# Kernel tuning notes

Measured on AMD Instinct MI355X. Metric: run time of the kernel, lower is better.

## Reference

```python
import jax, jax.numpy as jnp
import numpy as np

H = 64          # hidden_dim
L = 4           # num_layers
N_SENS = 32
OUT_DIM = 3
EPS = 1e-5


def _ln(x, g, b):
    m = jnp.mean(x, axis=-1, keepdims=True)
    v = jnp.var(x, axis=-1, keepdims=True)
    return (x - m) / jnp.sqrt(v + EPS) * g + b


def _gelu(x):
    return jax.nn.gelu(x, approximate=False)  # torch nn.GELU default (erf)


def setup_inputs() -> dict:
    key = jax.random.key(0)
    ks = jax.random.split(key, 12)
    B, T = 512, 2048
    s = 0.05
    return {
        "sensors": jax.random.normal(ks[0], (B, T, N_SENS), dtype=jnp.float32),
        # input_proj: Linear(n_sensors,H), LayerNorm(H), GELU, Linear(H,H)
        "W_in1": jax.random.normal(ks[1], (N_SENS, H), dtype=jnp.float32) * s,
        "b_in1": jnp.zeros((H,), jnp.float32),
        "ln1_g": jnp.ones((H,), jnp.float32),
        "ln1_b": jnp.zeros((H,), jnp.float32),
        "W_in2": jax.random.normal(ks[2], (H, H), dtype=jnp.float32) * s,
        "b_in2": jnp.zeros((H,), jnp.float32),
        # stacked LSTM cell gate weights: Linear(2H, 4H) per layer
        "Wg": jax.random.normal(ks[3], (L, 2 * H, 4 * H), dtype=jnp.float32) * s,
        "bg": jnp.zeros((L, 4 * H), jnp.float32),
        # output_proj: LayerNorm(H), Linear(H,H), GELU, Linear(H,out)
        "ln2_g": jnp.ones((H,), jnp.float32),
        "ln2_b": jnp.zeros((H,), jnp.float32),
        "W_out1": jax.random.normal(ks[4], (H, H), dtype=jnp.float32) * s,
        "b_out1": jnp.zeros((H,), jnp.float32),
        "W_out2": jax.random.normal(ks[5], (H, OUT_DIM), dtype=jnp.float32) * s,
        "b_out2": jnp.zeros((OUT_DIM,), jnp.float32),
    }


def _forward(sensors, W_in1, b_in1, ln1_g, ln1_b, W_in2, b_in2,
             Wg, bg, ln2_g, ln2_b, W_out1, b_out1, W_out2, b_out2):
    B, T, _ = sensors.shape
    # input projection (batched over B,T)
    x = _gelu(_ln(sensors @ W_in1 + b_in1, ln1_g, ln1_b)) @ W_in2 + b_in2  # [B,T,H]
    x_t = jnp.swapaxes(x, 0, 1)  # [T,B,H] for scan over time

    h0 = jnp.zeros((L, B, H), x.dtype)
    c0 = jnp.zeros((L, B, H), x.dtype)

    def step(carry, xt):
        h, c = carry  # [L,B,H]
        inp = xt
        hs, cs = [], []
        for l in range(L):  # fixed small layer loop
            combined = jnp.concatenate([inp, h[l]], axis=-1)  # [B,2H]
            gates = combined @ Wg[l] + bg[l]                   # [B,4H]
            i, f, g, o = jnp.split(gates, 4, axis=-1)
            c_new = jax.nn.sigmoid(f) * c[l] + jax.nn.sigmoid(i) * jnp.tanh(g)
            h_new = jax.nn.sigmoid(o) * jnp.tanh(c_new)
            hs.append(h_new)
            cs.append(c_new)
            inp = h_new
        return (jnp.stack(hs), jnp.stack(cs)), hs[-1]

    _, out_t = jax.lax.scan(step, (h0, c0), x_t)  # out_t: [T,B,H]
    out = jnp.swapaxes(out_t, 0, 1)  # [B,T,H]
    y = _gelu(_ln(out, ln2_g, ln2_b) @ W_out1 + b_out1) @ W_out2 + b_out2
    return y  # [B,T,OUT_DIM]


def reference(sensors, W_in1, b_in1, ln1_g, ln1_b, W_in2, b_in2,
              Wg, bg, ln2_g, ln2_b, W_out1, b_out1, W_out2, b_out2):
    return _forward(sensors, W_in1, b_in1, ln1_g, ln1_b, W_in2, b_in2,
                    Wg, bg, ln2_g, ln2_b, W_out1, b_out1, W_out2, b_out2)
```

## Files before the change

### kernel.cpp

```cpp
#include <hip/hip_runtime.h>
#include <math.h>

#define B_   512
#define T_   2048
#define H_   64
#define NS_  32
#define HH_  128
#define G4_  256
#define EPSF 1e-5f

typedef _Float16 half8 __attribute__((ext_vector_type(8)));
typedef _Float16 h4   __attribute__((ext_vector_type(4)));
typedef float    f32x4 __attribute__((ext_vector_type(4)));

__device__ __forceinline__ float gelu_f(float x) {
    return 0.5f * x * (1.0f + erff(x * 0.70710678118654752440f));
}
__device__ __forceinline__ float sigmoid_f(float x) {
    return 1.0f / (1.0f + __expf(-x));
}
__device__ __forceinline__ float tanh_f(float x) {
    return 1.0f - 2.0f / (__expf(2.0f * x) + 1.0f);
}

__global__ void __launch_bounds__(256) inproj_kernel(
    const float* __restrict__ sensors, const float* __restrict__ W1,
    const float* __restrict__ b1, const float* __restrict__ g1,
    const float* __restrict__ bb1, const float* __restrict__ W2,
    const float* __restrict__ b2, _Float16* __restrict__ seqh)
{
    __shared__ __align__(16) float W1l[NS_ * H_];
    __shared__ __align__(16) float W2l[H_ * H_];
    __shared__ float p1[H_], p2[H_], p3[H_], p4[H_];
    const int tid = threadIdx.x;
    {
        const float4* s1 = (const float4*)W1;
        float4* d1 = (float4*)W1l;
        for (int i = tid; i < NS_ * H_ / 4; i += 256) d1[i] = s1[i];
        const float4* s2 = (const float4*)W2;
        float4* d2 = (float4*)W2l;
        for (int i = tid; i < H_ * H_ / 4; i += 256) d2[i] = s2[i];
        if (tid < H_) { p1[tid] = b1[tid]; p2[tid] = g1[tid];
                        p3[tid] = bb1[tid]; p4[tid] = b2[tid]; }
    }
    __syncthreads();

    const long idx = (long)blockIdx.x * 256 + tid;
    const float* srow = sensors + idx * NS_;
    float sv[NS_];
    #pragma unroll
    for (int q = 0; q < NS_ / 4; ++q) {
        float4 v = *(const float4*)&srow[q * 4];
        sv[q*4+0] = v.x; sv[q*4+1] = v.y; sv[q*4+2] = v.z; sv[q*4+3] = v.w;
    }
    float t1[H_];
    #pragma unroll
    for (int jb = 0; jb < H_ / 4; ++jb) {
        float ax = p1[jb*4+0], ay = p1[jb*4+1], az = p1[jb*4+2], aw = p1[jb*4+3];
        #pragma unroll
        for (int k = 0; k < NS_; ++k) {
            float4 w = *(const float4*)&W1l[k * H_ + jb * 4];
            ax += sv[k]*w.x; ay += sv[k]*w.y; az += sv[k]*w.z; aw += sv[k]*w.w;
        }
        t1[jb*4+0] = ax; t1[jb*4+1] = ay; t1[jb*4+2] = az; t1[jb*4+3] = aw;
    }
    float mean = 0.f;
    #pragma unroll
    for (int j = 0; j < H_; ++j) mean += t1[j];
    mean *= (1.0f / H_);
    float var = 0.f;
    #pragma unroll
    for (int j = 0; j < H_; ++j) { float d = t1[j] - mean; var += d * d; }
    var *= (1.0f / H_);
    const float inv = rsqrtf(var + EPSF);
    #pragma unroll
    for (int j = 0; j < H_; ++j) {
        float nv = (t1[j] - mean) * inv * p2[j] + p3[j];
        t1[j] = gelu_f(nv);
    }
    _Float16* orow = seqh + idx * H_;
    for (int ob = 0; ob < H_ / 4; ++ob) {
        float ax = p4[ob*4+0], ay = p4[ob*4+1];
        float az = p4[ob*4+2], aw = p4[ob*4+3];
        #pragma unroll
        for (int j = 0; j < H_; ++j) {
            float4 w = *(const float4*)&W2l[j * H_ + ob * 4];
            ax += t1[j]*w.x; ay += t1[j]*w.y; az += t1[j]*w.z; aw += t1[j]*w.w;
        }
        h4 o; o[0] = (_Float16)ax; o[1] = (_Float16)ay;
              o[2] = (_Float16)az; o[3] = (_Float16)aw;
        *(h4*)&orow[ob * 4] = o;
    }
}

__global__ void __launch_bounds__(512, 2) lstm_fused_kernel(
    const float* __restrict__ Wg, const float* __restrict__ bg,
    const _Float16* __restrict__ xin,
    _Float16* __restrict__ h3out)
{
    __shared__ __align__(16) _Float16 combh[4][2][HH_];
    __shared__ __align__(8)  float gbuf[4][4][H_][2];

    const int tid  = threadIdx.x;
    const int wv   = tid >> 6;
    const int lane = tid & 63;
    const int l    = wv >> 1;
    const int half = wv & 1;
    const int L    = lane & 15;
    const int kgrp = lane >> 4;

    const float* W = Wg + (size_t)l * HH_ * G4_;
    half8 wf[4][8];
    #pragma unroll
    for (int kt = 0; kt < 4; ++kt) {
        #pragma unroll
        for (int nt = 0; nt < 8; ++nt) {
            const int col = half * 128 + nt * 16 + L;
            half8 f;
            #pragma unroll
            for (int j = 0; j < 8; ++j)
                f[j] = (_Float16)W[(kt * 32 + kgrp * 8 + j) * G4_ + col];
            wf[kt][nt] = f;
        }
    }
    float ba[8];
    #pragma unroll
    for (int nt = 0; nt < 8; ++nt)
        ba[nt] = bg[l * G4_ + half * 128 + nt * 16 + L];

    const int nl_l = tid >> 7;
    const int nrow = (tid >> 6) & 1;
    const int u    = tid & 63;
    const long nbase = ((long)(blockIdx.x * 2 + nrow)) * T_ * H_ + u;

    const int  xrow = lane >> 5;
    const int  xu   = half * 32 + (lane & 31);
    const long xbase = ((long)(blockIdx.x * 2 + xrow)) * T_ * H_ + xu;

    for (int i = tid; i < 4 * 2 * HH_ / 2; i += 512) ((float*)combh)[i] = 0.f;
    __syncthreads();
    if (l == 0) combh[0][xrow][xu] = xin[xbase];
    __syncthreads();

    float c_reg = 0.f;

    for (int s = 0; s < T_ + 3; ++s) {
        const bool mact = (s >= l) && (s - l < T_);
        const bool nact = (s >= nl_l) && (s - nl_l < T_);

        _Float16 xnext = (_Float16)0.f;
        if (l == 0 && s + 1 < T_)
            xnext = xin[xbase + (long)(s + 1) * H_];

        if (mact) {
            const _Float16* cp = &combh[l][lane & 1][0];
            half8 af[4];
            #pragma unroll
            for (int kt = 0; kt < 4; ++kt)
                af[kt] = *(const half8*)&cp[kt * 32 + kgrp * 8];

            f32x4 acc[8];
            #pragma unroll
            for (int nt = 0; nt < 8; ++nt)
                acc[nt] = (f32x4){ba[nt], ba[nt], ba[nt], ba[nt]};
            #pragma unroll
            for (int kt = 0; kt < 4; ++kt) {
                #pragma unroll
                for (int nt = 0; nt < 8; ++nt)
                    acc[nt] = __builtin_amdgcn_mfma_f32_16x16x32_f16(
                        af[kt], wf[kt][nt], acc[nt], 0, 0, 0);
            }
            if (lane < 16) {
                #pragma unroll
                for (int nt = 0; nt < 8; ++nt) {
                    const int col = half * 128 + nt * 16 + lane;
                    const int g   = col >> 6;
                    const int ug  = col & 63;
                    float2 v; v.x = acc[nt][0]; v.y = acc[nt][1];
                    *(float2*)&gbuf[l][g][ug][0] = v;
                }
            }
        }
        __syncthreads();

        if (nact) {
            const int t = s - nl_l;
            const float gi = gbuf[nl_l][0][u][nrow];
            const float gf = gbuf[nl_l][1][u][nrow];
            const float gg = gbuf[nl_l][2][u][nrow];
            const float go = gbuf[nl_l][3][u][nrow];
            c_reg = sigmoid_f(gf) * c_reg + sigmoid_f(gi) * tanh_f(gg);
            const float hn = sigmoid_f(go) * tanh_f(c_reg);
            const _Float16 hh = (_Float16)hn;
            combh[nl_l][nrow][64 + u] = hh;
            if (nl_l < 3) combh[nl_l + 1][nrow][u] = hh;
            else          h3out[nbase + (long)t * H_] = hh;
        }
        if (l == 0 && s + 1 < T_)
            combh[0][xrow][xu] = xnext;
        __syncthreads();
    }
}

__global__ void __launch_bounds__(256) outproj_kernel(
    const _Float16* __restrict__ h16,
    const float* __restrict__ g2, const float* __restrict__ b2,
    const float* __restrict__ W1, const float* __restrict__ b1,
    const float* __restrict__ W2, const float* __restrict__ b2o,
    float* __restrict__ y)
{
    __shared__ __align__(16) float W1l[H_ * H_];
    __shared__ __align__(16) float W2l[H_ * 4];
    __shared__ float pg[H_], pb[H_], pb1[H_];
    const int tid = threadIdx.x;
    {
        const float4* s1 = (const float4*)W1;
        float4* d1 = (float4*)W1l;
        for (int i = tid; i < H_ * H_ / 4; i += 256) d1[i] = s1[i];
        if (tid < H_) {
            pg[tid] = g2[tid]; pb[tid] = b2[tid]; pb1[tid] = b1[tid];
            float4 w; w.x = W2[tid*3+0]; w.y = W2[tid*3+1]; w.z = W2[tid*3+2]; w.w = 0.f;
            *(float4*)&W2l[tid * 4] = w;
        }
    }
    __syncthreads();

    const long idx = (long)blockIdx.x * 256 + tid;
    const _Float16* hrow = h16 + idx * H_;
    float hv[H_];
    #pragma unroll
    for (int q = 0; q < H_ / 8; ++q) {
        half8 v = *(const half8*)&hrow[q * 8];
        #pragma unroll
        for (int j = 0; j < 8; ++j) hv[q*8+j] = (float)v[j];
    }
    float mean = 0.f;
    #pragma unroll
    for (int j = 0; j < H_; ++j) mean += hv[j];
    mean *= (1.0f / H_);
    float var = 0.f;
    #pragma unroll
    for (int j = 0; j < H_; ++j) { float dd = hv[j] - mean; var += dd * dd; }
    var *= (1.0f / H_);
    const float inv = rsqrtf(var + EPSF);
    #pragma unroll
    for (int j = 0; j < H_; ++j) hv[j] = (hv[j] - mean) * inv * pg[j] + pb[j];

    float y0 = b2o[0], y1 = b2o[1], y2 = b2o[2];
    for (int ob = 0; ob < H_ / 4; ++ob) {
        float ax = pb1[ob*4+0], ay = pb1[ob*4+1];
        float az = pb1[ob*4+2], aw = pb1[ob*4+3];
        #pragma unroll
        for (int j = 0; j < H_; ++j) {
            float4 w = *(const float4*)&W1l[j * H_ + ob * 4];
            ax += hv[j]*w.x; ay += hv[j]*w.y; az += hv[j]*w.z; aw += hv[j]*w.w;
        }
        ax = gelu_f(ax); ay = gelu_f(ay); az = gelu_f(az); aw = gelu_f(aw);
        float4 wa = *(const float4*)&W2l[(ob*4+0) * 4];
        float4 wb = *(const float4*)&W2l[(ob*4+1) * 4];
        float4 wc = *(const float4*)&W2l[(ob*4+2) * 4];
        float4 wd = *(const float4*)&W2l[(ob*4+3) * 4];
        y0 += ax*wa.x + ay*wb.x + az*wc.x + aw*wd.x;
        y1 += ax*wa.y + ay*wb.y + az*wc.y + aw*wd.y;
        y2 += ax*wa.z + ay*wb.z + az*wc.z + aw*wd.z;
    }
    y[idx * 3 + 0] = y0;
    y[idx * 3 + 1] = y1;
    y[idx * 3 + 2] = y2;
}

extern "C" void kernel_launch(void* const* d_in, const int* in_sizes, int n_in,
                              void* d_out, int out_size, void* d_ws, size_t ws_size,
                              hipStream_t stream)
{
    const float* sensors = (const float*)d_in[0];
    const float* W_in1   = (const float*)d_in[1];
    const float* b_in1   = (const float*)d_in[2];
    const float* ln1_g   = (const float*)d_in[3];
    const float* ln1_b   = (const float*)d_in[4];
    const float* W_in2   = (const float*)d_in[5];
    const float* b_in2   = (const float*)d_in[6];
    const float* Wg      = (const float*)d_in[7];
    const float* bg      = (const float*)d_in[8];
    const float* ln2_g   = (const float*)d_in[9];
    const float* ln2_b   = (const float*)d_in[10];
    const float* W_out1  = (const float*)d_in[11];
    const float* b_out1  = (const float*)d_in[12];
    const float* W_out2  = (const float*)d_in[13];
    const float* b_out2  = (const float*)d_in[14];
    float* y = (float*)d_out;

    const size_t elems = (size_t)B_ * T_ * H_;
    _Float16* seqh = (_Float16*)d_ws;
    _Float16* h3   = (_Float16*)((char*)d_ws + elems * 2);

    inproj_kernel<<<B_ * T_ / 256, 256, 0, stream>>>(
        sensors, W_in1, b_in1, ln1_g, ln1_b, W_in2, b_in2, seqh);
    lstm_fused_kernel<<<B_ / 2, 512, 0, stream>>>(Wg, bg, seqh, h3);
    outproj_kernel<<<B_ * T_ / 256, 256, 0, stream>>>(
        h3, ln2_g, ln2_b, W_out1, b_out1, W_out2, b_out2, y);
}
```

Baseline: 3.082 ms.

## Split LSTM gate GEMM across 16 waves and stage x/h through chunked rings

The LSTM block grows from 512 to 1024 threads, so each layer's gate GEMM is split across four waves of 64 columns each instead of two waves of 128. That halves the per-wave MFMA chain on the serial critical path. Input x is now prefetched in 8-timestep chunks into a double-buffered shared ring with 16-byte loads. Layer-3 outputs are collected in a ring and written out in 16-byte vector stores by dedicated waves, replacing per-step scalar global loads and stores. The risks are heavier 1024-thread __syncthreads barriers on every step, lower occupancy per CU, and more shared memory.

```diff
diff --git a/kernel.cpp b/kernel.cpp
--- a/kernel.cpp
+++ b/kernel.cpp
@@ -93,112 +93,143 @@
     }
 }
 
-__global__ void __launch_bounds__(512, 2) lstm_fused_kernel(
+__global__ void __launch_bounds__(1024, 4) lstm_fused_kernel(
     const float* __restrict__ Wg, const float* __restrict__ bg,
     const _Float16* __restrict__ xin,
     _Float16* __restrict__ h3out)
 {
     __shared__ __align__(16) _Float16 combh[4][2][HH_];
-    __shared__ __align__(8)  float gbuf[4][4][H_][2];
+    __shared__ __align__(16) float    gbuf[4][2][4][H_];
+    __shared__ __align__(16) _Float16 xring[2][2][8][H_];
+    __shared__ __align__(16) _Float16 hring[2][2][8][H_];
 
     const int tid  = threadIdx.x;
     const int wv   = tid >> 6;
     const int lane = tid & 63;
-    const int l    = wv >> 1;
-    const int half = wv & 1;
+    const int l    = wv >> 2;
+    const int q    = wv & 3;
     const int L    = lane & 15;
     const int kgrp = lane >> 4;
+    const int arow = lane & 1;
 
     const float* W = Wg + (size_t)l * HH_ * G4_;
-    half8 wf[4][8];
+    half8 wf[4][4];
     #pragma unroll
     for (int kt = 0; kt < 4; ++kt) {
         #pragma unroll
-        for (int nt = 0; nt < 8; ++nt) {
-            const int col = half * 128 + nt * 16 + L;
+        for (int nt = 0; nt < 4; ++nt) {
             half8 f;
             #pragma unroll
             for (int j = 0; j < 8; ++j)
-                f[j] = (_Float16)W[(kt * 32 + kgrp * 8 + j) * G4_ + col];
+                f[j] = (_Float16)W[(kt * 32 + kgrp * 8 + j) * G4_
+                                   + q * 64 + nt * 16 + L];
             wf[kt][nt] = f;
         }
     }
-    float ba[8];
-    #pragma unroll
-    for (int nt = 0; nt < 8; ++nt)
-        ba[nt] = bg[l * G4_ + half * 128 + nt * 16 + L];
-
-    const int nl_l = tid >> 7;
-    const int nrow = (tid >> 6) & 1;
-    const int u    = tid & 63;
-    const long nbase = ((long)(blockIdx.x * 2 + nrow)) * T_ * H_ + u;
-
-    const int  xrow = lane >> 5;
-    const int  xu   = half * 32 + (lane & 31);
-    const long xbase = ((long)(blockIdx.x * 2 + xrow)) * T_ * H_ + xu;
-
-    for (int i = tid; i < 4 * 2 * HH_ / 2; i += 512) ((float*)combh)[i] = 0.f;
+    float ba[4];
+    #pragma unroll
+    for (int nt = 0; nt < 4; ++nt)
+        ba[nt] = bg[l * G4_ + q * 64 + nt * 16 + L];
+
+    const bool nlw  = tid < 512;
+    const int  nl_l = tid >> 7;
+    const int  nrow = (tid >> 6) & 1;
+    const int  u    = tid & 63;
+
+    const int xt  = lane >> 3;
+    const int xu8 = (lane & 7) * 8;
+
+    const bool xw   = (wv < 2);
+    const int  xrow = wv & 1;
+    const _Float16* xsrc =
+        xin + ((long)(blockIdx.x * 2 + xrow)) * T_ * H_ + xt * H_ + xu8;
+
+    const bool hw   = (wv >= 14);
+    const int  hrow = hw ? (wv - 14) : 0;
+    _Float16* hdst =
+        h3out + ((long)(blockIdx.x * 2 + hrow)) * T_ * H_ + xt * H_ + xu8;
+
+    if (tid < 512) ((float*)combh)[tid] = 0.f;
+    half8 xreg = {};
+    if (xw) xreg = *(const half8*)xsrc;
     __syncthreads();
-    if (l == 0) combh[0][xrow][xu] = xin[xbase];
+    if (xw) {
+        *(half8*)&xring[0][xrow][xt][xu8] = xreg;
+        xreg = *(const half8*)(xsrc + 8 * H_);
+    }
     __syncthreads();
 
     float c_reg = 0.f;
 
     for (int s = 0; s < T_ + 3; ++s) {
+        if (xw && (s & 7) == 0) {
+            const int c = s >> 3;
+            if (c + 1 < T_ / 8)
+                *(half8*)&xring[(c + 1) & 1][xrow][xt][xu8] = xreg;
+            if (c + 2 < T_ / 8)
+                xreg = *(const half8*)(xsrc + (long)(c + 2) * 8 * H_);
+        }
+        if (hw && s >= 11 && ((s - 3) & 7) == 0) {
+            const int cp = ((s - 3) >> 3) - 1;
+            half8 v = *(const half8*)&hring[cp & 1][hrow][xt][xu8];
+            *(half8*)(hdst + (long)cp * 8 * H_) = v;
+        }
+
         const bool mact = (s >= l) && (s - l < T_);
-        const bool nact = (s >= nl_l) && (s - nl_l < T_);
-
-        _Float16 xnext = (_Float16)0.f;
-        if (l == 0 && s + 1 < T_)
-            xnext = xin[xbase + (long)(s + 1) * H_];
-
         if (mact) {
-            const _Float16* cp = &combh[l][lane & 1][0];
-            half8 af[4];
+            const _Float16* px = (l == 0)
+                ? &xring[(s >> 3) & 1][arow][s & 7][0]
+                : &combh[l][arow][0];
+            const _Float16* ph = &combh[l][arow][64];
+            half8 af0 = *(const half8*)(px + kgrp * 8);
+            half8 af1 = *(const half8*)(px + 32 + kgrp * 8);
+            half8 af2 = *(const half8*)(ph + kgrp * 8);
+            half8 af3 = *(const half8*)(ph + 32 + kgrp * 8);
+
+            f32x4 acc[4];
             #pragma unroll
-            for (int kt = 0; kt < 4; ++kt)
-                af[kt] = *(const half8*)&cp[kt * 32 + kgrp * 8];
-
-            f32x4 acc[8];
-            #pragma unroll
-            for (int nt = 0; nt < 8; ++nt)
+            for (int nt = 0; nt < 4; ++nt)
                 acc[nt] = (f32x4){ba[nt], ba[nt], ba[nt], ba[nt]};
             #pragma unroll
-            for (int kt = 0; kt < 4; ++kt) {
-                #pragma unroll
-                for (int nt = 0; nt < 8; ++nt)
-                    acc[nt] = __builtin_amdgcn_mfma_f32_16x16x32_f16(
-                        af[kt], wf[kt][nt], acc[nt], 0, 0, 0);
+            for (int nt = 0; nt < 4; ++nt) {
+                acc[nt] = __builtin_amdgcn_mfma_f32_16x16x32_f16(af0, wf[0][nt], acc[nt], 0, 0, 0);
+                acc[nt] = __builtin_amdgcn_mfma_f32_16x16x32_f16(af1, wf[1][nt], acc[nt], 0, 0, 0);
+                acc[nt] = __builtin_amdgcn_mfma_f32_16x16x32_f16(af2, wf[2][nt], acc[nt], 0, 0, 0);
+                acc[nt] = __builtin_amdgcn_mfma_f32_16x16x32_f16(af3, wf[3][nt], acc[nt], 0, 0, 0);
             }
             if (lane < 16) {
                 #pragma unroll
-                for (int nt = 0; nt < 8; ++nt) {
-                    const int col = half * 128 + nt * 16 + lane;
-                    const int g   = col >> 6;
-                    const int ug  = col & 63;
-                    float2 v; v.x = acc[nt][0]; v.y = acc[nt][1];
-                    *(float2*)&gbuf[l][g][ug][0] = v;
+                for (int nt = 0; nt < 4; ++nt) {
+                    gbuf[l][0][q][nt * 16 + L] = acc[nt][0];
+                    gbuf[l][1][q][nt * 16 + L] = acc[nt][1];
                 }
             }
         }
         __syncthreads();
 
-        if (nact) {
-            const int t = s - nl_l;
-            const float gi = gbuf[nl_l][0][u][nrow];
-            const float gf = gbuf[nl_l][1][u][nrow];
-            const float gg = gbuf[nl_l][2][u][nrow];
-            const float go = gbuf[nl_l][3][u][nrow];
-            c_reg = sigmoid_f(gf) * c_reg + sigmoid_f(gi) * tanh_f(gg);
-            const float hn = sigmoid_f(go) * tanh_f(c_reg);
-            const _Float16 hh = (_Float16)hn;
-            combh[nl_l][nrow][64 + u] = hh;
-            if (nl_l < 3) combh[nl_l + 1][nrow][u] = hh;
-            else          h3out[nbase + (long)t * H_] = hh;
-        }
-        if (l == 0 && s + 1 < T_)
-            combh[0][xrow][xu] = xnext;
+        if (nlw) {
+            const bool nact = (s >= nl_l) && (s - nl_l < T_);
+            if (nact) {
+                const int t = s - nl_l;
+                const float gi = gbuf[nl_l][nrow][0][u];
+                const float gf = gbuf[nl_l][nrow][1][u];
+                const float gg = gbuf[nl_l][nrow][2][u];
+                const float go = gbuf[nl_l][nrow][3][u];
+                c_reg = sigmoid_f(gf) * c_reg + sigmoid_f(gi) * tanh_f(gg);
+                const float hn = sigmoid_f(go) * tanh_f(c_reg);
+                const _Float16 hh = (_Float16)hn;
+                combh[nl_l][nrow][64 + u] = hh;
+                if (nl_l < 3) combh[nl_l + 1][nrow][u] = hh;
+                else hring[(t >> 3) & 1][nrow][t & 7][u] = hh;
+            }
+        }
         __syncthreads();
+    }
+
+    if (hw) {
+        const int cp = T_ / 8 - 1;
+        half8 v = *(const half8*)&hring[cp & 1][hrow][xt][xu8];
+        *(half8*)(hdst + (long)cp * 8 * H_) = v;
     }
 }
 
@@ -296,7 +327,7 @@
 
     inproj_kernel<<<B_ * T_ / 256, 256, 0, stream>>>(
         sensors, W_in1, b_in1, ln1_g, ln1_b, W_in2, b_in2, seqh);
-    lstm_fused_kernel<<<B_ / 2, 512, 0, stream>>>(Wg, bg, seqh, h3);
+    lstm_fused_kernel<<<B_ / 2, 1024, 0, stream>>>(Wg, bg, seqh, h3);
     outproj_kernel<<<B_ * T_ / 256, 256, 0, stream>>>(
         h3, ln2_g, ln2_b, W_out1, b_out1, W_out2, b_out2, y);
 }
```

New measurement: 3.355 ms. 1.09x slower.
